# Optimization experiments

Measured on AMD Instinct MI355X. Metric: run time of the kernel, lower is better.

## Reference

```python
import jax, jax.numpy as jnp
import numpy as np

N_ATOMS = 50000
N_EDGES = 1_600_000
N_MOL = 500
HIDDEN = 128
FILTERS = 128
GAUSS = 50
LAYERS = 3
CUTOFF = 10.0
LOG2 = 0.6931471805599453


def ssp(x):
    # ShiftedSoftplus: softplus(x) - log(2)
    return jax.nn.softplus(x) - LOG2


def setup_inputs() -> dict:
    key = jax.random.key(0)
    ks = jax.random.split(key, 24)
    z = jax.random.randint(ks[0], (N_ATOMS,), 0, 100)
    pos = jax.random.uniform(ks[1], (N_ATOMS, 3), jnp.float32) * 5.0  # box keeps d < cutoff
    batch = jnp.sort(jax.random.randint(ks[2], (N_ATOMS,), 0, N_MOL))
    row = jax.random.randint(ks[3], (N_EDGES,), 0, N_ATOMS)
    off = jax.random.randint(ks[4], (N_EDGES,), 1, N_ATOMS)
    col = (row + off) % N_ATOMS  # guarantees row != col (no zero distances)
    edge_index = jnp.stack([row, col])
    def lin(k, fi, fo):
        return jax.random.normal(k, (fi, fo), jnp.float32) * (1.0 / np.sqrt(fi))
    emb = jax.random.normal(ks[5], (100, HIDDEN), jnp.float32)
    mlp1_w = jnp.stack([lin(jax.random.fold_in(ks[6], i), GAUSS, FILTERS) for i in range(LAYERS)])
    mlp1_b = jnp.zeros((LAYERS, FILTERS), jnp.float32)
    mlp2_w = jnp.stack([lin(jax.random.fold_in(ks[7], i), FILTERS, FILTERS) for i in range(LAYERS)])
    mlp2_b = jnp.zeros((LAYERS, FILTERS), jnp.float32)
    lin1_w = jnp.stack([lin(jax.random.fold_in(ks[8], i), HIDDEN, FILTERS) for i in range(LAYERS)])
    lin2_w = jnp.stack([lin(jax.random.fold_in(ks[9], i), FILTERS, HIDDEN) for i in range(LAYERS)])
    lin2_b = jnp.zeros((LAYERS, HIDDEN), jnp.float32)
    int_w = jnp.stack([lin(jax.random.fold_in(ks[10], i), HIDDEN, HIDDEN) for i in range(LAYERS)])
    int_b = jnp.zeros((LAYERS, HIDDEN), jnp.float32)
    out1_w = lin(ks[11], HIDDEN, HIDDEN // 2)
    out1_b = jnp.zeros((HIDDEN // 2,), jnp.float32)
    out2_w = lin(ks[12], HIDDEN // 2, 1)
    out2_b = jnp.zeros((1,), jnp.float32)
    return {"z": z, "pos": pos, "batch": batch, "edge_index": edge_index,
            "emb": emb, "mlp1_w": mlp1_w, "mlp1_b": mlp1_b, "mlp2_w": mlp2_w, "mlp2_b": mlp2_b,
            "lin1_w": lin1_w, "lin2_w": lin2_w, "lin2_b": lin2_b, "int_w": int_w, "int_b": int_b,
            "out1_w": out1_w, "out1_b": out1_b, "out2_w": out2_w, "out2_b": out2_b}


def reference(z, pos, batch, edge_index, emb, mlp1_w, mlp1_b, mlp2_w, mlp2_b,
              lin1_w, lin2_w, lin2_b, int_w, int_b, out1_w, out1_b, out2_w, out2_b):
    row, col = edge_index[0], edge_index[1]  # source j, target i
    d = jnp.linalg.norm(pos[row] - pos[col], axis=-1)  # [E]
    # GaussianSmearing
    offset = jnp.linspace(0.0, CUTOFF, GAUSS)
    coeff = -0.5 / (offset[1] - offset[0]) ** 2
    rbf = jnp.exp(coeff * (d[:, None] - offset[None, :]) ** 2)  # [E, GAUSS]
    # cosine cutoff
    C = 0.5 * (jnp.cos(d * jnp.pi / CUTOFF) + 1.0)  # [E]
    h = emb[z]  # [N, H]
    for l in range(LAYERS):
        W = ssp(rbf @ mlp1_w[l] + mlp1_b[l]) @ mlp2_w[l] + mlp2_b[l]  # [E, F]
        W = W * C[:, None]
        x = h @ lin1_w[l]                 # [N, F]
        msg = x[row] * W                  # gather from source, per-edge filter
        agg = jax.ops.segment_sum(msg, col, num_segments=N_ATOMS)  # scatter-add to targets
        x = agg @ lin2_w[l] + lin2_b[l]
        x = ssp(x)
        x = x @ int_w[l] + int_b[l]
        h = h + x                         # residual
    h = ssp(h @ out1_w + out1_b)
    h = h @ out2_w + out2_b               # [N, 1] per-atom energy
    out = jax.ops.segment_sum(h[:, 0], batch, num_segments=N_MOL)  # 'add' readout
    return out.reshape(-1)
```

## Files before the change

kernel.cpp:

```cpp
#include <hip/hip_runtime.h>
#include <math.h>

#define HID 128
#define NGAUSS 50
#define TBL 2048
#define TBL2 8192
#define DMAX 8.6605f
#define LDX 136

typedef _Float16 h2 __attribute__((ext_vector_type(2)));
typedef _Float16 h4 __attribute__((ext_vector_type(4)));
typedef _Float16 f16x8 __attribute__((ext_vector_type(8)));
typedef float f32x4 __attribute__((ext_vector_type(4)));

__device__ __forceinline__ float sspf(float x) {
  float ax = fabsf(x);
  return fmaxf(x, 0.0f) + log1pf(expf(-ax)) - 0.69314718055994530942f;
}

__global__ __launch_bounds__(128) void build_table_k(
    const float* __restrict__ w1, const float* __restrict__ b1,
    const float* __restrict__ w2, const float* __restrict__ b2,
    float* __restrict__ tab) {
  int l = blockIdx.x >> 11;
  int ti = blockIdx.x & (TBL - 1);
  int j = threadIdx.x;
  __shared__ float rbf[NGAUSS];
  __shared__ float v1[HID];
  const float step = DMAX / (float)(TBL - 1);
  float d = ti * step;
  if (j < NGAUSS) {
    const float gstep = 10.0f / 49.0f;
    const float gcoeff = -12.005f;
    float diff = d - j * gstep;
    rbf[j] = expf(gcoeff * diff * diff);
  }
  __syncthreads();
  float s = b1[l * HID + j];
  const float* w1p = w1 + l * NGAUSS * HID + j;
  for (int g = 0; g < NGAUSS; g++) s = fmaf(rbf[g], w1p[g * HID], s);
  v1[j] = sspf(s);
  __syncthreads();
  float s2 = b2[l * HID + j];
  const float* w2p = w2 + l * HID * HID + j;
  for (int k = 0; k < HID; k++) s2 = fmaf(v1[k], w2p[k * HID], s2);
  float C = 0.5f * (cosf(d * 0.3141592653589793f) + 1.0f);
  tab[((size_t)l * TBL + ti) * HID + j] = s2 * C;
}

__global__ __launch_bounds__(256) void upsample_k(
    const float* __restrict__ tab, _Float16* __restrict__ tabh) {
  int idx = blockIdx.x * 256 + threadIdx.x;
  if (idx >= 3 * TBL2 * HID) return;
  int ch = idx & 127;
  int i = (idx >> 7) & (TBL2 - 1);
  int l = idx >> 20;
  float t = (float)i * ((float)(TBL - 1) / (float)(TBL2 - 1));
  int i0 = min((int)t, TBL - 2);
  float f = t - (float)i0;
  const float* base = tab + ((size_t)l * TBL + i0) * HID + ch;
  tabh[idx] = (_Float16)fmaf(f, base[HID] - base[0], base[0]);
}

__global__ __launch_bounds__(256) void wtrans10_k(
    const float* __restrict__ lin1, const float* __restrict__ lin2,
    const float* __restrict__ intw, const float* __restrict__ out1w,
    _Float16* __restrict__ out) {
  int b = blockIdx.x;
  __shared__ _Float16 tile[128 * 130];
  int t = threadIdx.x;
  if (b < 9) {
    const float* src = (b < 3 ? lin1 : (b < 6 ? lin2 : intw)) + (size_t)(b % 3) * HID * HID;
    _Float16* dst = out + (size_t)b * HID * HID;
    for (int i = t; i < HID * HID; i += 256) tile[(i >> 7) * 130 + (i & 127)] = (_Float16)src[i];
    __syncthreads();
    for (int i = t; i < HID * HID; i += 256) dst[i] = tile[(i & 127) * 130 + (i >> 7)];
  } else {
    _Float16* dst = out + (size_t)9 * HID * HID;
    for (int i = t; i < 128 * 64; i += 256) tile[(i >> 6) * 66 + (i & 63)] = (_Float16)out1w[i];
    __syncthreads();
    for (int i = t; i < 64 * 128; i += 256) dst[i] = tile[(i & 127) * 66 + (i >> 7)];
  }
}

__global__ __launch_bounds__(256) void bcount_k(
    const int* __restrict__ col, int* __restrict__ bcount, int E, int nbuck) {
  __shared__ int hist[1024];
  int t = threadIdx.x;
  int e0 = blockIdx.x * 2048;
  for (int j = t; j < nbuck; j += 256) hist[j] = 0;
  __syncthreads();
#pragma unroll
  for (int u = 0; u < 8; u++) {
    int e = e0 + u * 256 + t;
    if (e < E) atomicAdd(&hist[col[e] >> 6], 1);
  }
  __syncthreads();
  for (int j = t; j < nbuck; j += 256)
    if (hist[j]) atomicAdd(&bcount[j], hist[j]);
}

__global__ __launch_bounds__(256) void bucket_scan_k(
    const int* __restrict__ bcount, int* __restrict__ bstart,
    int* __restrict__ bcur, int nbuck, int* __restrict__ starts, int N) {
  __shared__ int sh[256];
  int t = threadIdx.x;
  int chunk = (nbuck + 255) / 256;
  int b0 = t * chunk;
  int c[8];
  int s = 0;
  for (int j = 0; j < chunk; j++) {
    int idx = b0 + j;
    int v = (idx < nbuck) ? bcount[idx] : 0;
    c[j] = v;
    s += v;
  }
  sh[t] = s;
  __syncthreads();
  for (int o = 1; o < 256; o <<= 1) {
    int v = (t >= o) ? sh[t - o] : 0;
    __syncthreads();
    sh[t] += v;
    __syncthreads();
  }
  int p = (t == 0) ? 0 : sh[t - 1];
  for (int j = 0; j < chunk; j++) {
    int idx = b0 + j;
    if (idx < nbuck) {
      bstart[idx] = p;
      bcur[idx] = p;
      p += c[j];
    }
  }
  if (t == 255) {
    bstart[nbuck] = p;
    starts[N] = p;
  }
}

__global__ __launch_bounds__(256) void scatterA_k(
    const int* __restrict__ row, const int* __restrict__ col,
    const float* __restrict__ pos, int* __restrict__ bcur,
    unsigned long long* __restrict__ tmp, int E, int nbuck) {
  __shared__ int hist[1024];
  __shared__ int base[1024];
  int t = threadIdx.x;
  int e0 = blockIdx.x * 2048;
  for (int j = t; j < nbuck; j += 256) hist[j] = 0;
  __syncthreads();
  int bkt[8];
  int rnk[8];
  unsigned long long key[8];
#pragma unroll
  for (int u = 0; u < 8; u++) {
    int e = e0 + u * 256 + t;
    bkt[u] = -1;
    if (e < E) {
      int r = row[e], c = col[e];
      float dx = pos[r * 3 + 0] - pos[c * 3 + 0];
      float dy = pos[r * 3 + 1] - pos[c * 3 + 1];
      float dz = pos[r * 3 + 2] - pos[c * 3 + 2];
      float d = sqrtf(dx * dx + dy * dy + dz * dz);
      const float inv2 = (float)(TBL2 - 1) / DMAX;
      int q = min((int)(d * inv2 + 0.5f), TBL2 - 1);
      unsigned int pay = ((unsigned int)r << 13) | (unsigned int)q;
      key[u] = ((unsigned long long)pay << 6) | (unsigned long long)(c & 63);
      bkt[u] = c >> 6;
      rnk[u] = atomicAdd(&hist[bkt[u]], 1);
    }
  }
  __syncthreads();
  for (int j = t; j < nbuck; j += 256)
    base[j] = hist[j] ? atomicAdd(&bcur[j], hist[j]) : 0;
  __syncthreads();
#pragma unroll
  for (int u = 0; u < 8; u++)
    if (bkt[u] >= 0) tmp[(size_t)base[bkt[u]] + rnk[u]] = key[u];
}

__global__ __launch_bounds__(256) void scatterB_k(
    const unsigned long long* __restrict__ tmp, const int* __restrict__ bstart,
    int* __restrict__ starts, unsigned int* __restrict__ payload, int N) {
  int j = blockIdx.x;
  int t = threadIdx.x;
  __shared__ int cnt[64];
  __shared__ int cur[64];
  int rs = bstart[j], re = bstart[j + 1];
  if (t < 64) cnt[t] = 0;
  __syncthreads();
  for (int e = rs + t; e < re; e += 256)
    atomicAdd(&cnt[(int)(tmp[e] & 63)], 1);
  __syncthreads();
  if (t < 64) {
    int mine = cnt[t];
    int v = mine;
    for (int o = 1; o < 64; o <<= 1) {
      int u = __shfl_up(v, o, 64);
      if (t >= o) v += u;
    }
    int excl = v - mine;
    int c = j * 64 + t;
    if (c < N) starts[c] = rs + excl;
    cur[t] = rs + excl;
  }
  __syncthreads();
  for (int e = rs + t; e < re; e += 256) {
    unsigned long long k = tmp[e];
    int p = atomicAdd(&cur[(int)(k & 63)], 1);
    payload[p] = (unsigned int)(k >> 6);
  }
}

__global__ __launch_bounds__(256) void lin1_emb_k(
    const int* __restrict__ z, const float* __restrict__ emb,
    const _Float16* __restrict__ W1t, float* __restrict__ h,
    _Float16* __restrict__ x16, int N) {
  __shared__ __align__(16) _Float16 Xs[64 * LDX];
  __shared__ __align__(16) _Float16 Ws[128 * LDX];
  __shared__ int zi[64];
  int t = threadIdx.x;
  int a0 = blockIdx.x * 64;
  if (t < 64) zi[t] = (a0 + t < N) ? z[a0 + t] : 0;
  __syncthreads();
#pragma unroll
  for (int p = 0; p < 8; p++) {
    int fi = t + p * 256;
    int a = fi >> 5, kg = fi & 31;
    float4 v = make_float4(0.f, 0.f, 0.f, 0.f);
    if (a0 + a < N) {
      v = ((const float4*)emb)[(size_t)zi[a] * 32 + kg];
      ((float4*)h)[(size_t)(a0 + a) * 32 + kg] = v;
    }
    h4 o;
    o.x = (_Float16)v.x; o.y = (_Float16)v.y;
    o.z = (_Float16)v.z; o.w = (_Float16)v.w;
    *(h4*)&Xs[a * LDX + kg * 4] = o;
  }
#pragma unroll
  for (int p = 0; p < 8; p++) {
    int si = t + p * 256;
    int n = si >> 4, kg = si & 15;
    *(uint4*)&Ws[n * LDX + kg * 8] = ((const uint4*)W1t)[si];
  }
  __syncthreads();
  int lane = t & 63;
  int w = t >> 6;
  int mrow = lane & 15, quad = lane >> 4;
  f32x4 zero = {0.f, 0.f, 0.f, 0.f};
  f32x4 acc[8];
#pragma unroll
  for (int i = 0; i < 8; i++) acc[i] = zero;
#pragma unroll
  for (int kk = 0; kk < 4; kk++) {
    f16x8 af = *(const f16x8*)&Xs[(w * 16 + mrow) * LDX + kk * 32 + quad * 8];
#pragma unroll
    for (int nt = 0; nt < 8; nt++) {
      f16x8 bf = *(const f16x8*)&Ws[(nt * 16 + mrow) * LDX + kk * 32 + quad * 8];
      acc[nt] = __builtin_amdgcn_mfma_f32_16x16x32_f16(af, bf, acc[nt], 0, 0, 0);
    }
  }
  __syncthreads();
#pragma unroll
  for (int nt = 0; nt < 8; nt++)
#pragma unroll
    for (int r = 0; r < 4; r++)
      Xs[(w * 16 + quad * 4 + r) * LDX + nt * 16 + mrow] = (_Float16)acc[nt][r];
  __syncthreads();
#pragma unroll
  for (int p = 0; p < 4; p++) {
    int ci = t + p * 256;
    int a = ci >> 4, kg = ci & 15;
    if (a0 + a < N)
      ((uint4*)x16)[(size_t)(a0 + a) * 16 + kg] = *(uint4*)&Xs[a * LDX + kg * 8];
  }
}

__global__ __launch_bounds__(256) void fused_mid_k(
    const _Float16* __restrict__ agg16, const _Float16* __restrict__ W2t,
    const float* __restrict__ b2, const _Float16* __restrict__ W3t,
    const float* __restrict__ b3, float* __restrict__ h,
    const _Float16* __restrict__ W1nt, _Float16* __restrict__ x16, int N) {
  __shared__ __align__(16) _Float16 Xs[64 * LDX];
  __shared__ __align__(16) _Float16 Ws[128 * LDX];
  float* Fs = (float*)Ws;
  int t = threadIdx.x;
  int a0 = blockIdx.x * 64;
#pragma unroll
  for (int p = 0; p < 4; p++) {
    int ci = t + p * 256;
    int a = ci >> 4, kg = ci & 15;
    uint4 v = make_uint4(0, 0, 0, 0);
    if (a0 + a < N) v = ((const uint4*)agg16)[(size_t)(a0 + a) * 16 + kg];
    *(uint4*)&Xs[a * LDX + kg * 8] = v;
  }
#pragma unroll
  for (int p = 0; p < 8; p++) {
    int si = t + p * 256;
    int n = si >> 4, kg = si & 15;
    *(uint4*)&Ws[n * LDX + kg * 8] = ((const uint4*)W2t)[si];
  }
  __syncthreads();
  int lane = t & 63;
  int w = t >> 6;
  int mrow = lane & 15, quad = lane >> 4;
  f32x4 zero = {0.f, 0.f, 0.f, 0.f};
  f32x4 acc[8];
#pragma unroll
  for (int i = 0; i < 8; i++) acc[i] = zero;
#pragma unroll
  for (int kk = 0; kk < 4; kk++) {
    f16x8 af = *(const f16x8*)&Xs[(w * 16 + mrow) * LDX + kk * 32 + quad * 8];
#pragma unroll
    for (int nt = 0; nt < 8; nt++) {
      f16x8 bf = *(const f16x8*)&Ws[(nt * 16 + mrow) * LDX + kk * 32 + quad * 8];
      acc[nt] = __builtin_amdgcn_mfma_f32_16x16x32_f16(af, bf, acc[nt], 0, 0, 0);
    }
  }
  float b2r[8];
#pragma unroll
  for (int nt = 0; nt < 8; nt++) b2r[nt] = b2[nt * 16 + mrow];
  __syncthreads();
#pragma unroll
  for (int nt = 0; nt < 8; nt++)
#pragma unroll
    for (int r = 0; r < 4; r++)
      Xs[(w * 16 + quad * 4 + r) * LDX + nt * 16 + mrow] = (_Float16)sspf(acc[nt][r] + b2r[nt]);
#pragma unroll
  for (int p = 0; p < 8; p++) {
    int si = t + p * 256;
    int n = si >> 4, kg = si & 15;
    *(uint4*)&Ws[n * LDX + kg * 8] = ((const uint4*)W3t)[si];
  }
  __syncthreads();
#pragma unroll
  for (int i = 0; i < 8; i++) acc[i] = zero;
#pragma unroll
  for (int kk = 0; kk < 4; kk++) {
    f16x8 af = *(const f16x8*)&Xs[(w * 16 + mrow) * LDX + kk * 32 + quad * 8];
#pragma unroll
    for (int nt = 0; nt < 8; nt++) {
      f16x8 bf = *(const f16x8*)&Ws[(nt * 16 + mrow) * LDX + kk * 32 + quad * 8];
      acc[nt] = __builtin_amdgcn_mfma_f32_16x16x32_f16(af, bf, acc[nt], 0, 0, 0);
    }
  }
  float b3r[8];
#pragma unroll
  for (int nt = 0; nt < 8; nt++) b3r[nt] = b3[nt * 16 + mrow];
  __syncthreads();
#pragma unroll
  for (int nt = 0; nt < 8; nt++)
#pragma unroll
    for (int r = 0; r < 4; r++)
      Fs[(w * 16 + quad * 4 + r) * 132 + nt * 16 + mrow] = acc[nt][r] + b3r[nt];
  __syncthreads();
#pragma unroll
  for (int p = 0; p < 8; p++) {
    int ci = t + p * 256;
    int a = ci >> 5, kg = ci & 31;
    float4 v = *(float4*)&Fs[a * 132 + kg * 4];
    if (a0 + a < N) {
      float4 ho = ((const float4*)h)[(size_t)(a0 + a) * 32 + kg];
      v.x += ho.x; v.y += ho.y; v.z += ho.z; v.w += ho.w;
      ((float4*)h)[(size_t)(a0 + a) * 32 + kg] = v;
    }
    h4 o;
    o.x = (_Float16)v.x; o.y = (_Float16)v.y;
    o.z = (_Float16)v.z; o.w = (_Float16)v.w;
    *(h4*)&Xs[a * LDX + kg * 4] = o;
  }
  __syncthreads();
#pragma unroll
  for (int p = 0; p < 8; p++) {
    int si = t + p * 256;
    int n = si >> 4, kg = si & 15;
    *(uint4*)&Ws[n * LDX + kg * 8] = ((const uint4*)W1nt)[si];
  }
  __syncthreads();
#pragma unroll
  for (int i = 0; i < 8; i++) acc[i] = zero;
#pragma unroll
  for (int kk = 0; kk < 4; kk++) {
    f16x8 af = *(const f16x8*)&Xs[(w * 16 + mrow) * LDX + kk * 32 + quad * 8];
#pragma unroll
    for (int nt = 0; nt < 8; nt++) {
      f16x8 bf = *(const f16x8*)&Ws[(nt * 16 + mrow) * LDX + kk * 32 + quad * 8];
      acc[nt] = __builtin_amdgcn_mfma_f32_16x16x32_f16(af, bf, acc[nt], 0, 0, 0);
    }
  }
  __syncthreads();
#pragma unroll
  for (int nt = 0; nt < 8; nt++)
#pragma unroll
    for (int r = 0; r < 4; r++)
      Xs[(w * 16 + quad * 4 + r) * LDX + nt * 16 + mrow] = (_Float16)acc[nt][r];
  __syncthreads();
#pragma unroll
  for (int p = 0; p < 4; p++) {
    int ci = t + p * 256;
    int a = ci >> 4, kg = ci & 15;
    if (a0 + a < N)
      ((uint4*)x16)[(size_t)(a0 + a) * 16 + kg] = *(uint4*)&Xs[a * LDX + kg * 8];
  }
}

__global__ __launch_bounds__(256) void fused_last_k(
    const _Float16* __restrict__ agg16, const _Float16* __restrict__ W2t,
    const float* __restrict__ b2, const _Float16* __restrict__ W3t,
    const float* __restrict__ b3, const float* __restrict__ h,
    const _Float16* __restrict__ Wo1t, const float* __restrict__ o1b,
    const float* __restrict__ o2w, const float* __restrict__ o2b,
    const int* __restrict__ batch, float* __restrict__ out, int N) {
  __shared__ __align__(16) _Float16 Xs[64 * LDX];
  __shared__ __align__(16) _Float16 Ws[128 * LDX];
  float* Fs = (float*)Ws;
  int t = threadIdx.x;
  int a0 = blockIdx.x * 64;
#pragma unroll
  for (int p = 0; p < 4; p++) {
    int ci = t + p * 256;
    int a = ci >> 4, kg = ci & 15;
    uint4 v = make_uint4(0, 0, 0, 0);
    if (a0 + a < N) v = ((const uint4*)agg16)[(size_t)(a0 + a) * 16 + kg];
    *(uint4*)&Xs[a * LDX + kg * 8] = v;
  }
#pragma unroll
  for (int p = 0; p < 8; p++) {
    int si = t + p * 256;
    int n = si >> 4, kg = si & 15;
    *(uint4*)&Ws[n * LDX + kg * 8] = ((const uint4*)W2t)[si];
  }
  __syncthreads();
  int lane = t & 63;
  int w = t >> 6;
  int mrow = lane & 15, quad = lane >> 4;
  f32x4 zero = {0.f, 0.f, 0.f, 0.f};
  f32x4 acc[8];
#pragma unroll
  for (int i = 0; i < 8; i++) acc[i] = zero;
#pragma unroll
  for (int kk = 0; kk < 4; kk++) {
    f16x8 af = *(const f16x8*)&Xs[(w * 16 + mrow) * LDX + kk * 32 + quad * 8];
#pragma unroll
    for (int nt = 0; nt < 8; nt++) {
      f16x8 bf = *(const f16x8*)&Ws[(nt * 16 + mrow) * LDX + kk * 32 + quad * 8];
      acc[nt] = __builtin_amdgcn_mfma_f32_16x16x32_f16(af, bf, acc[nt], 0, 0, 0);
    }
  }
  float b2r[8];
#pragma unroll
  for (int nt = 0; nt < 8; nt++) b2r[nt] = b2[nt * 16 + mrow];
  __syncthreads();
#pragma unroll
  for (int nt = 0; nt < 8; nt++)
#pragma unroll
    for (int r = 0; r < 4; r++)
      Xs[(w * 16 + quad * 4 + r) * LDX + nt * 16 + mrow] = (_Float16)sspf(acc[nt][r] + b2r[nt]);
#pragma unroll
  for (int p = 0; p < 8; p++) {
    int si = t + p * 256;
    int n = si >> 4, kg = si & 15;
    *(uint4*)&Ws[n * LDX + kg * 8] = ((const uint4*)W3t)[si];
  }
  __syncthreads();
#pragma unroll
  for (int i = 0; i < 8; i++) acc[i] = zero;
#pragma unroll
  for (int kk = 0; kk < 4; kk++) {
    f16x8 af = *(const f16x8*)&Xs[(w * 16 + mrow) * LDX + kk * 32 + quad * 8];
#pragma unroll
    for (int nt = 0; nt < 8; nt++) {
      f16x8 bf = *(const f16x8*)&Ws[(nt * 16 + mrow) * LDX + kk * 32 + quad * 8];
      acc[nt] = __builtin_amdgcn_mfma_f32_16x16x32_f16(af, bf, acc[nt], 0, 0, 0);
    }
  }
  float b3r[8];
#pragma unroll
  for (int nt = 0; nt < 8; nt++) b3r[nt] = b3[nt * 16 + mrow];
  __syncthreads();
#pragma unroll
  for (int nt = 0; nt < 8; nt++)
#pragma unroll
    for (int r = 0; r < 4; r++)
      Fs[(w * 16 + quad * 4 + r) * 132 + nt * 16 + mrow] = acc[nt][r] + b3r[nt];
  __syncthreads();
#pragma unroll
  for (int p = 0; p < 8; p++) {
    int ci = t + p * 256;
    int a = ci >> 5, kg = ci & 31;
    float4 v = *(float4*)&Fs[a * 132 + kg * 4];
    if (a0 + a < N) {
      float4 ho = ((const float4*)h)[(size_t)(a0 + a) * 32 + kg];
      v.x += ho.x; v.y += ho.y; v.z += ho.z; v.w += ho.w;
    }
    h4 o;
    o.x = (_Float16)v.x; o.y = (_Float16)v.y;
    o.z = (_Float16)v.z; o.w = (_Float16)v.w;
    *(h4*)&Xs[a * LDX + kg * 4] = o;
  }
  __syncthreads();
#pragma unroll
  for (int p = 0; p < 4; p++) {
    int si = t + p * 256;
    int n = si >> 4, kg = si & 15;
    *(uint4*)&Ws[n * LDX + kg * 8] = ((const uint4*)Wo1t)[si];
  }
  __syncthreads();
#pragma unroll
  for (int i = 0; i < 4; i++) acc[i] = zero;
#pragma unroll
  for (int kk = 0; kk < 4; kk++) {
    f16x8 af = *(const f16x8*)&Xs[(w * 16 + mrow) * LDX + kk * 32 + quad * 8];
#pragma unroll
    for (int nt = 0; nt < 4; nt++) {
      f16x8 bf = *(const f16x8*)&Ws[(nt * 16 + mrow) * LDX + kk * 32 + quad * 8];
      acc[nt] = __builtin_amdgcn_mfma_f32_16x16x32_f16(af, bf, acc[nt], 0, 0, 0);
    }
  }
  float o2b0 = o2b[0];
  float ss[4] = {0.f, 0.f, 0.f, 0.f};
#pragma unroll
  for (int nt = 0; nt < 4; nt++) {
    float bb = o1b[nt * 16 + mrow];
    float ww = o2w[nt * 16 + mrow];
#pragma unroll
    for (int r = 0; r < 4; r++) ss[r] += sspf(acc[nt][r] + bb) * ww;
  }
#pragma unroll
  for (int r = 0; r < 4; r++) {
    ss[r] += __shfl_xor(ss[r], 1);
    ss[r] += __shfl_xor(ss[r], 2);
    ss[r] += __shfl_xor(ss[r], 4);
    ss[r] += __shfl_xor(ss[r], 8);
    int a = a0 + w * 16 + quad * 4 + r;
    if (mrow == 0 && a < N) atomicAdd(&out[batch[a]], ss[r] + o2b0);
  }
}

__global__ __launch_bounds__(256) void aggregate_k(
    const int* __restrict__ starts, const unsigned int* __restrict__ payload,
    const _Float16* __restrict__ x16, const _Float16* __restrict__ tabh,
    _Float16* __restrict__ agg16, int N) {
  int a = blockIdx.x * 4 + (threadIdx.x >> 6);
  if (a >= N) return;
  int lane = threadIdx.x & 63;
  int half = lane >> 5;
  int sl = lane & 31;
  int s = starts[a], e_end = starts[a + 1];
  float4 acc0 = make_float4(0.f, 0.f, 0.f, 0.f);
  float4 acc1 = make_float4(0.f, 0.f, 0.f, 0.f);
  auto do_edge = [&](unsigned int p, float4& acc) {
    int tq = (int)(p & 8191u);
    int r = (int)(p >> 13);
    h4 tw = *(const h4*)&tabh[(size_t)tq * HID + sl * 4];
    h4 xr = *(const h4*)&x16[(size_t)r * HID + sl * 4];
    acc.x = fmaf((float)xr.x, (float)tw.x, acc.x);
    acc.y = fmaf((float)xr.y, (float)tw.y, acc.y);
    acc.z = fmaf((float)xr.z, (float)tw.z, acc.z);
    acc.w = fmaf((float)xr.w, (float)tw.w, acc.w);
  };
  int i = s;
  for (; i + 8 <= e_end; i += 8) {
    unsigned int p0 = payload[i + half];
    unsigned int p1 = payload[i + 2 + half];
    unsigned int p2 = payload[i + 4 + half];
    unsigned int p3 = payload[i + 6 + half];
    do_edge(p0, acc0);
    do_edge(p1, acc1);
    do_edge(p2, acc0);
    do_edge(p3, acc1);
  }
  for (; i < e_end; i += 2) {
    int e = i + half;
    if (e < e_end) do_edge(payload[e], acc0);
  }
  acc0.x += acc1.x; acc0.y += acc1.y; acc0.z += acc1.z; acc0.w += acc1.w;
  acc0.x += __shfl_xor(acc0.x, 32);
  acc0.y += __shfl_xor(acc0.y, 32);
  acc0.z += __shfl_xor(acc0.z, 32);
  acc0.w += __shfl_xor(acc0.w, 32);
  if (half == 0) {
    h4 o;
    o.x = (_Float16)acc0.x; o.y = (_Float16)acc0.y;
    o.z = (_Float16)acc0.z; o.w = (_Float16)acc0.w;
    *(h4*)&agg16[(size_t)a * HID + sl * 4] = o;
  }
}

extern "C" void kernel_launch(void* const* d_in, const int* in_sizes, int n_in,
                              void* d_out, int out_size, void* d_ws, size_t ws_size,
                              hipStream_t stream) {
  const int* z = (const int*)d_in[0];
  const float* pos = (const float*)d_in[1];
  const int* batch = (const int*)d_in[2];
  const int* eidx = (const int*)d_in[3];
  const float* emb = (const float*)d_in[4];
  const float* mlp1_w = (const float*)d_in[5];
  const float* mlp1_b = (const float*)d_in[6];
  const float* mlp2_w = (const float*)d_in[7];
  const float* mlp2_b = (const float*)d_in[8];
  const float* lin1_w = (const float*)d_in[9];
  const float* lin2_w = (const float*)d_in[10];
  const float* lin2_b = (const float*)d_in[11];
  const float* int_w = (const float*)d_in[12];
  const float* int_b = (const float*)d_in[13];
  const float* out1_w = (const float*)d_in[14];
  const float* out1_b = (const float*)d_in[15];
  const float* out2_w = (const float*)d_in[16];
  const float* out2_b = (const float*)d_in[17];
  float* out = (float*)d_out;

  const int N = in_sizes[0];
  const int E = in_sizes[3] / 2;
  const int* row = eidx;
  const int* col = eidx + E;
  const int nbuck = (N + 63) / 64;

  char* ws = (char*)d_ws;
  size_t off = 0;
  auto alloc = [&](size_t bytes) -> void* {
    void* p = ws + off;
    off = (off + bytes + 255) & ~(size_t)255;
    return p;
  };
  float* h = (float*)alloc((size_t)N * HID * 4);
  _Float16* x16 = (_Float16*)alloc((size_t)N * HID * 2);
  size_t agg_bytes = (size_t)N * HID * 2;
  size_t tmp_bytes = (size_t)E * 8 + 16;
  void* agg_union = alloc(agg_bytes > tmp_bytes ? agg_bytes : tmp_bytes);
  _Float16* agg16 = (_Float16*)agg_union;
  unsigned long long* tmp = (unsigned long long*)agg_union;
  unsigned int* payload = (unsigned int*)alloc((size_t)E * 4 + 16);
  int* starts = (int*)alloc((size_t)(N + 1) * 4);
  int* bcount = (int*)alloc((size_t)nbuck * 4);
  int* bstart = (int*)alloc((size_t)(nbuck + 1) * 4);
  int* bcur = (int*)alloc((size_t)nbuck * 4);
  float* tab = (float*)alloc((size_t)3 * TBL * HID * 4);
  _Float16* tabh = (_Float16*)alloc((size_t)3 * TBL2 * HID * 2);
  _Float16* Wt10 = (_Float16*)alloc((size_t)10 * HID * HID * 2);
  (void)ws_size;

  hipMemsetAsync(bcount, 0, (size_t)nbuck * 4, stream);
  hipMemsetAsync(out, 0, (size_t)out_size * 4, stream);

  build_table_k<<<3 * TBL, 128, 0, stream>>>(mlp1_w, mlp1_b, mlp2_w, mlp2_b, tab);
  upsample_k<<<(3 * TBL2 * HID + 255) / 256, 256, 0, stream>>>(tab, tabh);
  wtrans10_k<<<10, 256, 0, stream>>>(lin1_w, lin2_w, int_w, out1_w, Wt10);
  bcount_k<<<(E + 2047) / 2048, 256, 0, stream>>>(col, bcount, E, nbuck);
  bucket_scan_k<<<1, 256, 0, stream>>>(bcount, bstart, bcur, nbuck, starts, N);
  scatterA_k<<<(E + 2047) / 2048, 256, 0, stream>>>(row, col, pos, bcur, tmp, E, nbuck);
  scatterB_k<<<nbuck, 256, 0, stream>>>(tmp, bstart, starts, payload, N);

  int gemm_grid = (N + 63) / 64;
  lin1_emb_k<<<gemm_grid, 256, 0, stream>>>(z, emb, Wt10, h, x16, N);
  for (int l = 0; l < 2; l++) {
    aggregate_k<<<(N + 3) / 4, 256, 0, stream>>>(starts, payload, x16,
                                                 tabh + (size_t)l * TBL2 * HID, agg16, N);
    fused_mid_k<<<gemm_grid, 256, 0, stream>>>(
        agg16, Wt10 + (size_t)(3 + l) * HID * HID, lin2_b + (size_t)l * HID,
        Wt10 + (size_t)(6 + l) * HID * HID, int_b + (size_t)l * HID, h,
        Wt10 + (size_t)(l + 1) * HID * HID, x16, N);
  }
  aggregate_k<<<(N + 3) / 4, 256, 0, stream>>>(starts, payload, x16,
                                               tabh + (size_t)2 * TBL2 * HID, agg16, N);
  fused_last_k<<<gemm_grid, 256, 0, stream>>>(
      agg16, Wt10 + (size_t)5 * HID * HID, lin2_b + (size_t)2 * HID,
      Wt10 + (size_t)8 * HID * HID, int_b + (size_t)2 * HID, h,
      Wt10 + (size_t)9 * HID * HID, out1_b, out2_w, out2_b, batch, out, N);
}
```

Baseline: 586.8 us.

## Load MFMA operands directly from global memory and drop shared weight staging

The per-atom dense kernels (lin1_emb, fused_mid, final) stop staging the weight matrices and input rows through shared memory. Each wave now reads its A fragments and the B weight fragments straight from global memory (weights stay L2/L1 resident), and the block-wide __syncthreads are removed. Each wave reuses only its own 16-row slice of Xs for the activation handoff between GEMMs. Outputs and the h residual are written element-wise from the MFMA layout rather than through coalesced shared-memory transposes. This cuts LDS use and barriers, which can raise occupancy, at the cost of redundant global weight reads per wave and less coalesced stores.

```diff
diff --git a/kernel.cpp b/kernel.cpp
--- a/kernel.cpp
+++ b/kernel.cpp
@@ -8,7 +8,6 @@
 #define DMAX 8.6605f
 #define LDX 136
 
-typedef _Float16 h2 __attribute__((ext_vector_type(2)));
 typedef _Float16 h4 __attribute__((ext_vector_type(4)));
 typedef _Float16 f16x8 __attribute__((ext_vector_type(8)));
 typedef float f32x4 __attribute__((ext_vector_type(4)));
@@ -215,63 +214,52 @@
     const int* __restrict__ z, const float* __restrict__ emb,
     const _Float16* __restrict__ W1t, float* __restrict__ h,
     _Float16* __restrict__ x16, int N) {
-  __shared__ __align__(16) _Float16 Xs[64 * LDX];
-  __shared__ __align__(16) _Float16 Ws[128 * LDX];
-  __shared__ int zi[64];
-  int t = threadIdx.x;
+  int t = threadIdx.x;
+  int lane = t & 63, w = t >> 6;
+  int mrow = lane & 15, quad = lane >> 4;
   int a0 = blockIdx.x * 64;
-  if (t < 64) zi[t] = (a0 + t < N) ? z[a0 + t] : 0;
-  __syncthreads();
-#pragma unroll
-  for (int p = 0; p < 8; p++) {
-    int fi = t + p * 256;
-    int a = fi >> 5, kg = fi & 31;
-    float4 v = make_float4(0.f, 0.f, 0.f, 0.f);
-    if (a0 + a < N) {
-      v = ((const float4*)emb)[(size_t)zi[a] * 32 + kg];
-      ((float4*)h)[(size_t)(a0 + a) * 32 + kg] = v;
-    }
-    h4 o;
-    o.x = (_Float16)v.x; o.y = (_Float16)v.y;
-    o.z = (_Float16)v.z; o.w = (_Float16)v.w;
-    *(h4*)&Xs[a * LDX + kg * 4] = o;
-  }
-#pragma unroll
-  for (int p = 0; p < 8; p++) {
-    int si = t + p * 256;
-    int n = si >> 4, kg = si & 15;
-    *(uint4*)&Ws[n * LDX + kg * 8] = ((const uint4*)W1t)[si];
-  }
-  __syncthreads();
-  int lane = t & 63;
-  int w = t >> 6;
-  int mrow = lane & 15, quad = lane >> 4;
+  int am = a0 + w * 16 + mrow;
+  int amc = min(am, N - 1);
+  int zz = z[amc];
+  const float* er = emb + (size_t)zz * HID;
+  f16x8 af[4];
+#pragma unroll
+  for (int kk = 0; kk < 4; kk++) {
+    float4 e0 = *(const float4*)(er + kk * 32 + quad * 8);
+    float4 e1 = *(const float4*)(er + kk * 32 + quad * 8 + 4);
+    if (am < N) {
+      *(float4*)(h + (size_t)am * HID + kk * 32 + quad * 8) = e0;
+      *(float4*)(h + (size_t)am * HID + kk * 32 + quad * 8 + 4) = e1;
+    }
+    f16x8 a8;
+    a8[0] = (_Float16)e0.x; a8[1] = (_Float16)e0.y;
+    a8[2] = (_Float16)e0.z; a8[3] = (_Float16)e0.w;
+    a8[4] = (_Float16)e1.x; a8[5] = (_Float16)e1.y;
+    a8[6] = (_Float16)e1.z; a8[7] = (_Float16)e1.w;
+    af[kk] = a8;
+  }
   f32x4 zero = {0.f, 0.f, 0.f, 0.f};
   f32x4 acc[8];
 #pragma unroll
   for (int i = 0; i < 8; i++) acc[i] = zero;
 #pragma unroll
   for (int kk = 0; kk < 4; kk++) {
-    f16x8 af = *(const f16x8*)&Xs[(w * 16 + mrow) * LDX + kk * 32 + quad * 8];
-#pragma unroll
-    for (int nt = 0; nt < 8; nt++) {
-      f16x8 bf = *(const f16x8*)&Ws[(nt * 16 + mrow) * LDX + kk * 32 + quad * 8];
-      acc[nt] = __builtin_amdgcn_mfma_f32_16x16x32_f16(af, bf, acc[nt], 0, 0, 0);
-    }
-  }
-  __syncthreads();
-#pragma unroll
-  for (int nt = 0; nt < 8; nt++)
-#pragma unroll
-    for (int r = 0; r < 4; r++)
-      Xs[(w * 16 + quad * 4 + r) * LDX + nt * 16 + mrow] = (_Float16)acc[nt][r];
-  __syncthreads();
-#pragma unroll
-  for (int p = 0; p < 4; p++) {
-    int ci = t + p * 256;
-    int a = ci >> 4, kg = ci & 15;
-    if (a0 + a < N)
-      ((uint4*)x16)[(size_t)(a0 + a) * 16 + kg] = *(uint4*)&Xs[a * LDX + kg * 8];
+    f16x8 bf[8];
+#pragma unroll
+    for (int nt = 0; nt < 8; nt++)
+      bf[nt] = *(const f16x8*)(W1t + (size_t)(nt * 16 + mrow) * HID + kk * 32 + quad * 8);
+#pragma unroll
+    for (int nt = 0; nt < 8; nt++)
+      acc[nt] = __builtin_amdgcn_mfma_f32_16x16x32_f16(af[kk], bf[nt], acc[nt], 0, 0, 0);
+  }
+#pragma unroll
+  for (int nt = 0; nt < 8; nt++) {
+    int colv = nt * 16 + mrow;
+#pragma unroll
+    for (int r = 0; r < 4; r++) {
+      int a = a0 + w * 16 + quad * 4 + r;
+      if (a < N) x16[(size_t)a * HID + colv] = (_Float16)acc[nt][r];
+    }
   }
 }
 
@@ -281,125 +269,91 @@
     const float* __restrict__ b3, float* __restrict__ h,
     const _Float16* __restrict__ W1nt, _Float16* __restrict__ x16, int N) {
   __shared__ __align__(16) _Float16 Xs[64 * LDX];
-  __shared__ __align__(16) _Float16 Ws[128 * LDX];
-  float* Fs = (float*)Ws;
-  int t = threadIdx.x;
+  int t = threadIdx.x;
+  int lane = t & 63, w = t >> 6;
+  int mrow = lane & 15, quad = lane >> 4;
   int a0 = blockIdx.x * 64;
-#pragma unroll
-  for (int p = 0; p < 4; p++) {
-    int ci = t + p * 256;
-    int a = ci >> 4, kg = ci & 15;
-    uint4 v = make_uint4(0, 0, 0, 0);
-    if (a0 + a < N) v = ((const uint4*)agg16)[(size_t)(a0 + a) * 16 + kg];
-    *(uint4*)&Xs[a * LDX + kg * 8] = v;
-  }
-#pragma unroll
-  for (int p = 0; p < 8; p++) {
-    int si = t + p * 256;
-    int n = si >> 4, kg = si & 15;
-    *(uint4*)&Ws[n * LDX + kg * 8] = ((const uint4*)W2t)[si];
-  }
-  __syncthreads();
-  int lane = t & 63;
-  int w = t >> 6;
-  int mrow = lane & 15, quad = lane >> 4;
+  int am = min(a0 + w * 16 + mrow, N - 1);
+  f16x8 af[4];
+  const _Float16* arow = agg16 + (size_t)am * HID;
+#pragma unroll
+  for (int kk = 0; kk < 4; kk++)
+    af[kk] = *(const f16x8*)(arow + kk * 32 + quad * 8);
   f32x4 zero = {0.f, 0.f, 0.f, 0.f};
   f32x4 acc[8];
 #pragma unroll
   for (int i = 0; i < 8; i++) acc[i] = zero;
 #pragma unroll
   for (int kk = 0; kk < 4; kk++) {
-    f16x8 af = *(const f16x8*)&Xs[(w * 16 + mrow) * LDX + kk * 32 + quad * 8];
-#pragma unroll
-    for (int nt = 0; nt < 8; nt++) {
-      f16x8 bf = *(const f16x8*)&Ws[(nt * 16 + mrow) * LDX + kk * 32 + quad * 8];
-      acc[nt] = __builtin_amdgcn_mfma_f32_16x16x32_f16(af, bf, acc[nt], 0, 0, 0);
-    }
-  }
-  float b2r[8];
-#pragma unroll
-  for (int nt = 0; nt < 8; nt++) b2r[nt] = b2[nt * 16 + mrow];
-  __syncthreads();
-#pragma unroll
-  for (int nt = 0; nt < 8; nt++)
+    f16x8 bf[8];
+#pragma unroll
+    for (int nt = 0; nt < 8; nt++)
+      bf[nt] = *(const f16x8*)(W2t + (size_t)(nt * 16 + mrow) * HID + kk * 32 + quad * 8);
+#pragma unroll
+    for (int nt = 0; nt < 8; nt++)
+      acc[nt] = __builtin_amdgcn_mfma_f32_16x16x32_f16(af[kk], bf[nt], acc[nt], 0, 0, 0);
+  }
+#pragma unroll
+  for (int nt = 0; nt < 8; nt++) {
+    float bb = b2[nt * 16 + mrow];
 #pragma unroll
     for (int r = 0; r < 4; r++)
-      Xs[(w * 16 + quad * 4 + r) * LDX + nt * 16 + mrow] = (_Float16)sspf(acc[nt][r] + b2r[nt]);
-#pragma unroll
-  for (int p = 0; p < 8; p++) {
-    int si = t + p * 256;
-    int n = si >> 4, kg = si & 15;
-    *(uint4*)&Ws[n * LDX + kg * 8] = ((const uint4*)W3t)[si];
-  }
-  __syncthreads();
+      Xs[(w * 16 + quad * 4 + r) * LDX + nt * 16 + mrow] = (_Float16)sspf(acc[nt][r] + bb);
+  }
+#pragma unroll
+  for (int kk = 0; kk < 4; kk++)
+    af[kk] = *(const f16x8*)&Xs[(w * 16 + mrow) * LDX + kk * 32 + quad * 8];
 #pragma unroll
   for (int i = 0; i < 8; i++) acc[i] = zero;
 #pragma unroll
   for (int kk = 0; kk < 4; kk++) {
-    f16x8 af = *(const f16x8*)&Xs[(w * 16 + mrow) * LDX + kk * 32 + quad * 8];
-#pragma unroll
-    for (int nt = 0; nt < 8; nt++) {
-      f16x8 bf = *(const f16x8*)&Ws[(nt * 16 + mrow) * LDX + kk * 32 + quad * 8];
-      acc[nt] = __builtin_amdgcn_mfma_f32_16x16x32_f16(af, bf, acc[nt], 0, 0, 0);
-    }
-  }
-  float b3r[8];
-#pragma unroll
-  for (int nt = 0; nt < 8; nt++) b3r[nt] = b3[nt * 16 + mrow];
-  __syncthreads();
-#pragma unroll
-  for (int nt = 0; nt < 8; nt++)
-#pragma unroll
-    for (int r = 0; r < 4; r++)
-      Fs[(w * 16 + quad * 4 + r) * 132 + nt * 16 + mrow] = acc[nt][r] + b3r[nt];
-  __syncthreads();
-#pragma unroll
-  for (int p = 0; p < 8; p++) {
-    int ci = t + p * 256;
-    int a = ci >> 5, kg = ci & 31;
-    float4 v = *(float4*)&Fs[a * 132 + kg * 4];
-    if (a0 + a < N) {
-      float4 ho = ((const float4*)h)[(size_t)(a0 + a) * 32 + kg];
-      v.x += ho.x; v.y += ho.y; v.z += ho.z; v.w += ho.w;
-      ((float4*)h)[(size_t)(a0 + a) * 32 + kg] = v;
-    }
-    h4 o;
-    o.x = (_Float16)v.x; o.y = (_Float16)v.y;
-    o.z = (_Float16)v.z; o.w = (_Float16)v.w;
-    *(h4*)&Xs[a * LDX + kg * 4] = o;
-  }
-  __syncthreads();
-#pragma unroll
-  for (int p = 0; p < 8; p++) {
-    int si = t + p * 256;
-    int n = si >> 4, kg = si & 15;
-    *(uint4*)&Ws[n * LDX + kg * 8] = ((const uint4*)W1nt)[si];
-  }
-  __syncthreads();
+    f16x8 bf[8];
+#pragma unroll
+    for (int nt = 0; nt < 8; nt++)
+      bf[nt] = *(const f16x8*)(W3t + (size_t)(nt * 16 + mrow) * HID + kk * 32 + quad * 8);
+#pragma unroll
+    for (int nt = 0; nt < 8; nt++)
+      acc[nt] = __builtin_amdgcn_mfma_f32_16x16x32_f16(af[kk], bf[nt], acc[nt], 0, 0, 0);
+  }
+#pragma unroll
+  for (int nt = 0; nt < 8; nt++) {
+    int colv = nt * 16 + mrow;
+    float bb = b3[colv];
+#pragma unroll
+    for (int r = 0; r < 4; r++) {
+      int a = a0 + w * 16 + quad * 4 + r;
+      float v = acc[nt][r] + bb;
+      if (a < N) {
+        float* hp = h + (size_t)a * HID + colv;
+        v += *hp;
+        *hp = v;
+      }
+      Xs[(w * 16 + quad * 4 + r) * LDX + colv] = (_Float16)v;
+    }
+  }
+#pragma unroll
+  for (int kk = 0; kk < 4; kk++)
+    af[kk] = *(const f16x8*)&Xs[(w * 16 + mrow) * LDX + kk * 32 + quad * 8];
 #pragma unroll
   for (int i = 0; i < 8; i++) acc[i] = zero;
 #pragma unroll
   for (int kk = 0; kk < 4; kk++) {
-    f16x8 af = *(const f16x8*)&Xs[(w * 16 + mrow) * LDX + kk * 32 + quad * 8];
-#pragma unroll
-    for (int nt = 0; nt < 8; nt++) {
-      f16x8 bf = *(const f16x8*)&Ws[(nt * 16 + mrow) * LDX + kk * 32 + quad * 8];
-      acc[nt] = __builtin_amdgcn_mfma_f32_16x16x32_f16(af, bf, acc[nt], 0, 0, 0);
-    }
-  }
-  __syncthreads();
-#pragma unroll
-  for (int nt = 0; nt < 8; nt++)
-#pragma unroll
-    for (int r = 0; r < 4; r++)
-      Xs[(w * 16 + quad * 4 + r) * LDX + nt * 16 + mrow] = (_Float16)acc[nt][r];
-  __syncthreads();
-#pragma unroll
-  for (int p = 0; p < 4; p++) {
-    int ci = t + p * 256;
-    int a = ci >> 4, kg = ci & 15;
-    if (a0 + a < N)
-      ((uint4*)x16)[(size_t)(a0 + a) * 16 + kg] = *(uint4*)&Xs[a * LDX + kg * 8];
+    f16x8 bf[8];
+#pragma unroll
+    for (int nt = 0; nt < 8; nt++)
+      bf[nt] = *(const f16x8*)(W1nt + (size_t)(nt * 16 + mrow) * HID + kk * 32 + quad * 8);
+#pragma unroll
+    for (int nt = 0; nt < 8; nt++)
+      acc[nt] = __builtin_amdgcn_mfma_f32_16x16x32_f16(af[kk], bf[nt], acc[nt], 0, 0, 0);
+  }
+#pragma unroll
+  for (int nt = 0; nt < 8; nt++) {
+    int colv = nt * 16 + mrow;
+#pragma unroll
+    for (int r = 0; r < 4; r++) {
+      int a = a0 + w * 16 + quad * 4 + r;
+      if (a < N) x16[(size_t)a * HID + colv] = (_Float16)acc[nt][r];
+    }
   }
 }
 
@@ -411,110 +365,78 @@
     const float* __restrict__ o2w, const float* __restrict__ o2b,
     const int* __restrict__ batch, float* __restrict__ out, int N) {
   __shared__ __align__(16) _Float16 Xs[64 * LDX];
-  __shared__ __align__(16) _Float16 Ws[128 * LDX];
-  float* Fs = (float*)Ws;
-  int t = threadIdx.x;
+  int t = threadIdx.x;
+  int lane = t & 63, w = t >> 6;
+  int mrow = lane & 15, quad = lane >> 4;
   int a0 = blockIdx.x * 64;
-#pragma unroll
-  for (int p = 0; p < 4; p++) {
-    int ci = t + p * 256;
-    int a = ci >> 4, kg = ci & 15;
-    uint4 v = make_uint4(0, 0, 0, 0);
-    if (a0 + a < N) v = ((const uint4*)agg16)[(size_t)(a0 + a) * 16 + kg];
-    *(uint4*)&Xs[a * LDX + kg * 8] = v;
-  }
-#pragma unroll
-  for (int p = 0; p < 8; p++) {
-    int si = t + p * 256;
-    int n = si >> 4, kg = si & 15;
-    *(uint4*)&Ws[n * LDX + kg * 8] = ((const uint4*)W2t)[si];
-  }
-  __syncthreads();
-  int lane = t & 63;
-  int w = t >> 6;
-  int mrow = lane & 15, quad = lane >> 4;
+  int am = min(a0 + w * 16 + mrow, N - 1);
+  f16x8 af[4];
+  const _Float16* arow = agg16 + (size_t)am * HID;
+#pragma unroll
+  for (int kk = 0; kk < 4; kk++)
+    af[kk] = *(const f16x8*)(arow + kk * 32 + quad * 8);
   f32x4 zero = {0.f, 0.f, 0.f, 0.f};
   f32x4 acc[8];
 #pragma unroll
   for (int i = 0; i < 8; i++) acc[i] = zero;
 #pragma unroll
   for (int kk = 0; kk < 4; kk++) {
-    f16x8 af = *(const f16x8*)&Xs[(w * 16 + mrow) * LDX + kk * 32 + quad * 8];
-#pragma unroll
-    for (int nt = 0; nt < 8; nt++) {
-      f16x8 bf = *(const f16x8*)&Ws[(nt * 16 + mrow) * LDX + kk * 32 + quad * 8];
-      acc[nt] = __builtin_amdgcn_mfma_f32_16x16x32_f16(af, bf, acc[nt], 0, 0, 0);
-    }
-  }
-  float b2r[8];
-#pragma unroll
-  for (int nt = 0; nt < 8; nt++) b2r[nt] = b2[nt * 16 + mrow];
-  __syncthreads();
-#pragma unroll
-  for (int nt = 0; nt < 8; nt++)
+    f16x8 bf[8];
+#pragma unroll
+    for (int nt = 0; nt < 8; nt++)
+      bf[nt] = *(const f16x8*)(W2t + (size_t)(nt * 16 + mrow) * HID + kk * 32 + quad * 8);
+#pragma unroll
+    for (int nt = 0; nt < 8; nt++)
+      acc[nt] = __builtin_amdgcn_mfma_f32_16x16x32_f16(af[kk], bf[nt], acc[nt], 0, 0, 0);
+  }
+#pragma unroll
+  for (int nt = 0; nt < 8; nt++) {
+    float bb = b2[nt * 16 + mrow];
 #pragma unroll
     for (int r = 0; r < 4; r++)
-      Xs[(w * 16 + quad * 4 + r) * LDX + nt * 16 + mrow] = (_Float16)sspf(acc[nt][r] + b2r[nt]);
-#pragma unroll
-  for (int p = 0; p < 8; p++) {
-    int si = t + p * 256;
-    int n = si >> 4, kg = si & 15;
-    *(uint4*)&Ws[n * LDX + kg * 8] = ((const uint4*)W3t)[si];
-  }
-  __syncthreads();
+      Xs[(w * 16 + quad * 4 + r) * LDX + nt * 16 + mrow] = (_Float16)sspf(acc[nt][r] + bb);
+  }
+#pragma unroll
+  for (int kk = 0; kk < 4; kk++)
+    af[kk] = *(const f16x8*)&Xs[(w * 16 + mrow) * LDX + kk * 32 + quad * 8];
 #pragma unroll
   for (int i = 0; i < 8; i++) acc[i] = zero;
 #pragma unroll
   for (int kk = 0; kk < 4; kk++) {
-    f16x8 af = *(const f16x8*)&Xs[(w * 16 + mrow) * LDX + kk * 32 + quad * 8];
-#pragma unroll
-    for (int nt = 0; nt < 8; nt++) {
-      f16x8 bf = *(const f16x8*)&Ws[(nt * 16 + mrow) * LDX + kk * 32 + quad * 8];
-      acc[nt] = __builtin_amdgcn_mfma_f32_16x16x32_f16(af, bf, acc[nt], 0, 0, 0);
-    }
-  }
-  float b3r[8];
-#pragma unroll
-  for (int nt = 0; nt < 8; nt++) b3r[nt] = b3[nt * 16 + mrow];
-  __syncthreads();
-#pragma unroll
-  for (int nt = 0; nt < 8; nt++)
-#pragma unroll
-    for (int r = 0; r < 4; r++)
-      Fs[(w * 16 + quad * 4 + r) * 132 + nt * 16 + mrow] = acc[nt][r] + b3r[nt];
-  __syncthreads();
-#pragma unroll
-  for (int p = 0; p < 8; p++) {
-    int ci = t + p * 256;
-    int a = ci >> 5, kg = ci & 31;
-    float4 v = *(float4*)&Fs[a * 132 + kg * 4];
-    if (a0 + a < N) {
-      float4 ho = ((const float4*)h)[(size_t)(a0 + a) * 32 + kg];
-      v.x += ho.x; v.y += ho.y; v.z += ho.z; v.w += ho.w;
-    }
-    h4 o;
-    o.x = (_Float16)v.x; o.y = (_Float16)v.y;
-    o.z = (_Float16)v.z; o.w = (_Float16)v.w;
-    *(h4*)&Xs[a * LDX + kg * 4] = o;
-  }
-  __syncthreads();
-#pragma unroll
-  for (int p = 0; p < 4; p++) {
-    int si = t + p * 256;
-    int n = si >> 4, kg = si & 15;
-    *(uint4*)&Ws[n * LDX + kg * 8] = ((const uint4*)Wo1t)[si];
-  }
-  __syncthreads();
+    f16x8 bf[8];
+#pragma unroll
+    for (int nt = 0; nt < 8; nt++)
+      bf[nt] = *(const f16x8*)(W3t + (size_t)(nt * 16 + mrow) * HID + kk * 32 + quad * 8);
+#pragma unroll
+    for (int nt = 0; nt < 8; nt++)
+      acc[nt] = __builtin_amdgcn_mfma_f32_16x16x32_f16(af[kk], bf[nt], acc[nt], 0, 0, 0);
+  }
+#pragma unroll
+  for (int nt = 0; nt < 8; nt++) {
+    int colv = nt * 16 + mrow;
+    float bb = b3[colv];
+#pragma unroll
+    for (int r = 0; r < 4; r++) {
+      int a = a0 + w * 16 + quad * 4 + r;
+      float v = acc[nt][r] + bb;
+      if (a < N) v += h[(size_t)a * HID + colv];
+      Xs[(w * 16 + quad * 4 + r) * LDX + colv] = (_Float16)v;
+    }
+  }
+#pragma unroll
+  for (int kk = 0; kk < 4; kk++)
+    af[kk] = *(const f16x8*)&Xs[(w * 16 + mrow) * LDX + kk * 32 + quad * 8];
 #pragma unroll
   for (int i = 0; i < 4; i++) acc[i] = zero;
 #pragma unroll
   for (int kk = 0; kk < 4; kk++) {
-    f16x8 af = *(const f16x8*)&Xs[(w * 16 + mrow) * LDX + kk * 32 + quad * 8];
-#pragma unroll
-    for (int nt = 0; nt < 4; nt++) {
-      f16x8 bf = *(const f16x8*)&Ws[(nt * 16 + mrow) * LDX + kk * 32 + quad * 8];
-      acc[nt] = __builtin_amdgcn_mfma_f32_16x16x32_f16(af, bf, acc[nt], 0, 0, 0);
-    }
+    f16x8 bf[4];
+#pragma unroll
+    for (int nt = 0; nt < 4; nt++)
+      bf[nt] = *(const f16x8*)(Wo1t + (size_t)(nt * 16 + mrow) * HID + kk * 32 + quad * 8);
+#pragma unroll
+    for (int nt = 0; nt < 4; nt++)
+      acc[nt] = __builtin_amdgcn_mfma_f32_16x16x32_f16(af[kk], bf[nt], acc[nt], 0, 0, 0);
   }
   float o2b0 = o2b[0];
   float ss[4] = {0.f, 0.f, 0.f, 0.f};
```

Result: slower. 658.2 us (+12.2%).
